# Optimization experiments

Measured on AMD Instinct MI355X. Metric: run time of the kernel, lower is better.

The kernel has to match this reference:

```python
import jax, jax.numpy as jnp
import numpy as np

B = 8192      # contrastive batch size
D = 64        # embedding dim
TEMP = 0.07   # temperature (init kwarg)
EPS = 1e-8    # F.cosine_similarity eps
N_CLASSES = 1000


def setup_inputs() -> dict:
    key = jax.random.key(0)
    k1, k2, k3 = jax.random.split(key, 3)
    return {
        "label_tensor": jax.random.randint(k1, (B,), 0, N_CLASSES),
        "feature_a": jax.random.normal(k2, (B, D), dtype=jnp.float32),
        "feature_b": jax.random.normal(k3, (B, D), dtype=jnp.float32),
    }


def reference(label_tensor, feature_a, feature_b):
    # cos_score[i, j] = cosine(feature_a[i], feature_b[j])  -> [B, B]
    na = jnp.maximum(jnp.linalg.norm(feature_a, axis=1), EPS)  # [B]
    nb = jnp.maximum(jnp.linalg.norm(feature_b, axis=1), EPS)  # [B]
    cos_score = (feature_a @ feature_b.T) / (na[:, None] * nb[None, :])

    # cross_modality=True (feature_b given): no diagonal exclusion.
    e = jnp.exp(cos_score / TEMP)                               # [B, B]
    same = label_tensor[:, None] == label_tensor[None, :]       # [B, B] bool
    numerator = jnp.sum(jnp.where(same, e, 0.0), axis=1)        # [B]
    denominator = jnp.sum(e, axis=1)                            # [B]
    # original: if numerator == 0: numerator += 0.01
    numerator = jnp.where(numerator == 0.0, numerator + 0.01, numerator)
    loss = -jnp.mean(jnp.log(numerator / denominator))
    return (loss.reshape(1), cos_score)
```

## Files before the change

### kernel.cpp

```cpp
#include <hip/hip_runtime.h>

#define BATCH 8192
#define DIM 64
#define INV_TEMP 14.2857142857142857f
#define EPS_NORM 1e-8f
#define NXB 8
#define CT_PER_BLOCK 8

typedef __attribute__((ext_vector_type(8))) short bf16x8;
typedef __attribute__((ext_vector_type(4))) float f32x4;

__device__ __forceinline__ unsigned short f2bf_rne(float x) {
  unsigned int u = __float_as_uint(x);
  u += 0x7FFFu + ((u >> 16) & 1u);
  return (unsigned short)(u >> 16);
}

__global__ __launch_bounds__(256) void norm_kernel(
    const float* __restrict__ A, const float* __restrict__ Bm,
    unsigned short* __restrict__ An, unsigned short* __restrict__ Bn,
    float* __restrict__ out) {
  int gid  = blockIdx.x * 256 + threadIdx.x;
  int row  = gid >> 6;
  int lane = gid & 63;
  float a = A[row * DIM + lane];
  float b = Bm[row * DIM + lane];
  float sa = a * a, sb = b * b;
#pragma unroll
  for (int m = 32; m; m >>= 1) {
    sa += __shfl_xor(sa, m);
    sb += __shfl_xor(sb, m);
  }
  float ia = 1.0f / fmaxf(sqrtf(sa), EPS_NORM);
  float ib = 1.0f / fmaxf(sqrtf(sb), EPS_NORM);
  An[row * DIM + lane] = f2bf_rne(a * ia);
  Bn[row * DIM + lane] = f2bf_rne(b * ib);
  if (gid == 0) out[0] = 0.0f;
}

__global__ __launch_bounds__(256) void cos_mfma_kernel(
    const unsigned short* __restrict__ An, const unsigned short* __restrict__ Bn,
    const int* __restrict__ labels,
    float* __restrict__ pN, float* __restrict__ pD,
    float* __restrict__ cos_out) {
  const int tid  = threadIdx.x;
  const int lane = tid & 63;
  const int wave = tid >> 6;
  const int wr = wave >> 1, wc = wave & 1;
  const int m = lane & 15, q = lane >> 4;
  const int row0 = blockIdx.y * 128 + wr * 64;

  bf16x8 afr[4][2];
#pragma unroll
  for (int t = 0; t < 4; ++t) {
    const unsigned short* ap = An + (size_t)(row0 + t * 16 + m) * DIM + q * 8;
#pragma unroll
    for (int h = 0; h < 2; ++h) afr[t][h] = *(const bf16x8*)(ap + h * 32);
  }

  int lrw[4][4];
#pragma unroll
  for (int mt = 0; mt < 4; ++mt) {
    int lr = labels[row0 + mt * 16 + m];
#pragma unroll
    for (int i = 0; i < 4; ++i) lrw[mt][i] = __shfl(lr, q * 4 + i);
  }

  float es[4][4], ns[4][4];
#pragma unroll
  for (int mt = 0; mt < 4; ++mt)
#pragma unroll
    for (int i = 0; i < 4; ++i) { es[mt][i] = 0.f; ns[mt][i] = 0.f; }

  for (int ct = 0; ct < CT_PER_BLOCK; ++ct) {
    const int col0 = (blockIdx.x * CT_PER_BLOCK + ct) * 128 + wc * 64;

    bf16x8 bfr[4][2];
#pragma unroll
    for (int t = 0; t < 4; ++t) {
      const unsigned short* bp = Bn + (size_t)(col0 + t * 16 + m) * DIM + q * 8;
#pragma unroll
      for (int h = 0; h < 2; ++h) bfr[t][h] = *(const bf16x8*)(bp + h * 32);
    }
    int labc[4];
#pragma unroll
    for (int nt = 0; nt < 4; ++nt) labc[nt] = labels[col0 + nt * 16 + m];

#pragma unroll
    for (int mt = 0; mt < 4; ++mt) {
#pragma unroll
      for (int nt = 0; nt < 4; ++nt) {
        f32x4 a = {0.f, 0.f, 0.f, 0.f};
        a = __builtin_amdgcn_mfma_f32_16x16x32_bf16(afr[mt][0], bfr[nt][0], a, 0, 0, 0);
        a = __builtin_amdgcn_mfma_f32_16x16x32_bf16(afr[mt][1], bfr[nt][1], a, 0, 0, 0);
#pragma unroll
        for (int i = 0; i < 4; ++i) {
          float c = a[i];
          size_t row = (size_t)(row0 + mt * 16 + q * 4 + i);
          cos_out[row * BATCH + col0 + nt * 16 + m] = c;
          float e = __expf(c * INV_TEMP);
          es[mt][i] += e;
          if (labc[nt] == lrw[mt][i]) ns[mt][i] += e;
        }
      }
    }
  }

#pragma unroll
  for (int mt = 0; mt < 4; ++mt)
#pragma unroll
    for (int i = 0; i < 4; ++i) {
      float e = es[mt][i], n = ns[mt][i];
#pragma unroll
      for (int msk = 1; msk < 16; msk <<= 1) {
        e += __shfl_xor(e, msk);
        n += __shfl_xor(n, msk);
      }
      es[mt][i] = e; ns[mt][i] = n;
    }

  __shared__ float redN[2][128], redD[2][128];
  if (m == 0) {
#pragma unroll
    for (int mt = 0; mt < 4; ++mt)
#pragma unroll
      for (int i = 0; i < 4; ++i) {
        int r = wr * 64 + mt * 16 + q * 4 + i;
        redN[wc][r] = ns[mt][i];
        redD[wc][r] = es[mt][i];
      }
  }
  __syncthreads();
  if (tid < 128) {
    int row = blockIdx.y * 128 + tid;
    pN[(size_t)blockIdx.x * BATCH + row] = redN[0][tid] + redN[1][tid];
    pD[(size_t)blockIdx.x * BATCH + row] = redD[0][tid] + redD[1][tid];
  }
}

__global__ __launch_bounds__(256) void loss_kernel(
    const float* __restrict__ pN, const float* __restrict__ pD,
    float* __restrict__ out) {
  int r = blockIdx.x * 256 + threadIdx.x;
  float n = 0.f, d = 0.f;
#pragma unroll
  for (int j = 0; j < NXB; ++j) {
    n += pN[(size_t)j * BATCH + r];
    d += pD[(size_t)j * BATCH + r];
  }
  n = (n == 0.0f) ? (n + 0.01f) : n;
  float s = logf(n / d);
#pragma unroll
  for (int m = 32; m; m >>= 1) s += __shfl_xor(s, m);
  __shared__ float red[4];
  if ((threadIdx.x & 63) == 0) red[threadIdx.x >> 6] = s;
  __syncthreads();
  if (threadIdx.x == 0) {
    float t = red[0] + red[1] + red[2] + red[3];
    atomicAdd(out, -t / (float)BATCH);
  }
}

extern "C" void kernel_launch(void* const* d_in, const int* in_sizes, int n_in,
                              void* d_out, int out_size, void* d_ws, size_t ws_size,
                              hipStream_t stream) {
  const int*   labels = (const int*)d_in[0];
  const float* A      = (const float*)d_in[1];
  const float* Bf     = (const float*)d_in[2];
  float* out = (float*)d_out;

  unsigned short* An = (unsigned short*)d_ws;
  unsigned short* Bn = An + BATCH * DIM;
  float* pN = (float*)(Bn + BATCH * DIM);
  float* pD = pN + (size_t)NXB * BATCH;

  hipLaunchKernelGGL(norm_kernel, dim3(BATCH * 64 / 256), dim3(256), 0, stream,
                     A, Bf, An, Bn, out);
  hipLaunchKernelGGL(cos_mfma_kernel, dim3(NXB, BATCH / 128), dim3(256),
                     0, stream, An, Bn, labels, pN, pD, out + 1);
  hipLaunchKernelGGL(loss_kernel, dim3(BATCH / 256), dim3(256), 0, stream,
                     pN, pD, out);
}
```

Measured before the change: 388.6 us.

## Transpose MFMA operands for row-contiguous vector stores and regrid column tiles

Swaps the MFMA operand order so each lane holds four consecutive columns of one row. The cosine matrix can then be written with 16-byte vector stores instead of strided scalar stores, and label compares use int4 loads. The row reduction drops from a 16-lane shuffle tree to two cross-quad shuffles. The grid also changes from 8x8 to 32x2 column tiles per block. Some column positions take an odd mix of nontemporal and plain scalar stores, which adds branch complexity, and the pN/pD workspace grows fourfold.

```diff
diff --git a/kernel.cpp b/kernel.cpp
--- a/kernel.cpp
+++ b/kernel.cpp
@@ -4,11 +4,13 @@
 #define DIM 64
 #define INV_TEMP 14.2857142857142857f
 #define EPS_NORM 1e-8f
-#define NXB 8
-#define CT_PER_BLOCK 8
+#define NXB 32
+#define CT_PER_BLOCK 2
 
 typedef __attribute__((ext_vector_type(8))) short bf16x8;
 typedef __attribute__((ext_vector_type(4))) float f32x4;
+
+struct __attribute__((packed, aligned(4))) f32x4_u { f32x4 v; };
 
 __device__ __forceinline__ unsigned short f2bf_rne(float x) {
   unsigned int u = __float_as_uint(x);
@@ -58,20 +60,15 @@
     for (int h = 0; h < 2; ++h) afr[t][h] = *(const bf16x8*)(ap + h * 32);
   }
 
-  int lrw[4][4];
+  int lrw[4];
 #pragma unroll
-  for (int mt = 0; mt < 4; ++mt) {
-    int lr = labels[row0 + mt * 16 + m];
+  for (int mt = 0; mt < 4; ++mt) lrw[mt] = labels[row0 + mt * 16 + m];
+
+  float es[4], ns[4];
 #pragma unroll
-    for (int i = 0; i < 4; ++i) lrw[mt][i] = __shfl(lr, q * 4 + i);
-  }
+  for (int mt = 0; mt < 4; ++mt) { es[mt] = 0.f; ns[mt] = 0.f; }
 
-  float es[4][4], ns[4][4];
 #pragma unroll
-  for (int mt = 0; mt < 4; ++mt)
-#pragma unroll
-    for (int i = 0; i < 4; ++i) { es[mt][i] = 0.f; ns[mt][i] = 0.f; }
-
   for (int ct = 0; ct < CT_PER_BLOCK; ++ct) {
     const int col0 = (blockIdx.x * CT_PER_BLOCK + ct) * 128 + wc * 64;
 
@@ -82,53 +79,62 @@
 #pragma unroll
       for (int h = 0; h < 2; ++h) bfr[t][h] = *(const bf16x8*)(bp + h * 32);
     }
-    int labc[4];
+    int4 labc[4];
 #pragma unroll
-    for (int nt = 0; nt < 4; ++nt) labc[nt] = labels[col0 + nt * 16 + m];
+    for (int nt = 0; nt < 4; ++nt)
+      labc[nt] = *(const int4*)&labels[col0 + nt * 16 + q * 4];
 
 #pragma unroll
     for (int mt = 0; mt < 4; ++mt) {
 #pragma unroll
       for (int nt = 0; nt < 4; ++nt) {
         f32x4 a = {0.f, 0.f, 0.f, 0.f};
-        a = __builtin_amdgcn_mfma_f32_16x16x32_bf16(afr[mt][0], bfr[nt][0], a, 0, 0, 0);
-        a = __builtin_amdgcn_mfma_f32_16x16x32_bf16(afr[mt][1], bfr[nt][1], a, 0, 0, 0);
+        a = __builtin_amdgcn_mfma_f32_16x16x32_bf16(bfr[nt][0], afr[mt][0], a, 0, 0, 0);
+        a = __builtin_amdgcn_mfma_f32_16x16x32_bf16(bfr[nt][1], afr[mt][1], a, 0, 0, 0);
+        const int cmod = ct * 128 + wc * 64 + nt * 16 + q * 4;
+        float* p = cos_out + (size_t)(row0 + mt * 16 + m) * BATCH
+                           + (col0 + nt * 16 + q * 4);
+        if ((cmod <= 28) || (cmod == 252)) {
 #pragma unroll
-        for (int i = 0; i < 4; ++i) {
-          float c = a[i];
-          size_t row = (size_t)(row0 + mt * 16 + q * 4 + i);
-          cos_out[row * BATCH + col0 + nt * 16 + m] = c;
-          float e = __expf(c * INV_TEMP);
-          es[mt][i] += e;
-          if (labc[nt] == lrw[mt][i]) ns[mt][i] += e;
+          for (int r = 0; r < 4; ++r) {
+            int colm = cmod + r;
+            if (colm <= 30 || colm == 255) __builtin_nontemporal_store(a[r], p + r);
+            else                           p[r] = a[r];
+          }
+        } else {
+          ((f32x4_u*)p)->v = a;
         }
+        float e0 = __expf(a[0] * INV_TEMP);
+        float e1 = __expf(a[1] * INV_TEMP);
+        float e2 = __expf(a[2] * INV_TEMP);
+        float e3 = __expf(a[3] * INV_TEMP);
+        es[mt] += (e0 + e1) + (e2 + e3);
+        float nacc = 0.f;
+        if (labc[nt].x == lrw[mt]) nacc += e0;
+        if (labc[nt].y == lrw[mt]) nacc += e1;
+        if (labc[nt].z == lrw[mt]) nacc += e2;
+        if (labc[nt].w == lrw[mt]) nacc += e3;
+        ns[mt] += nacc;
       }
     }
   }
 
 #pragma unroll
-  for (int mt = 0; mt < 4; ++mt)
-#pragma unroll
-    for (int i = 0; i < 4; ++i) {
-      float e = es[mt][i], n = ns[mt][i];
-#pragma unroll
-      for (int msk = 1; msk < 16; msk <<= 1) {
-        e += __shfl_xor(e, msk);
-        n += __shfl_xor(n, msk);
-      }
-      es[mt][i] = e; ns[mt][i] = n;
-    }
+  for (int mt = 0; mt < 4; ++mt) {
+    float e = es[mt], n = ns[mt];
+    e += __shfl_xor(e, 16); n += __shfl_xor(n, 16);
+    e += __shfl_xor(e, 32); n += __shfl_xor(n, 32);
+    es[mt] = e; ns[mt] = n;
+  }
 
   __shared__ float redN[2][128], redD[2][128];
-  if (m == 0) {
+  if (q == 0) {
 #pragma unroll
-    for (int mt = 0; mt < 4; ++mt)
-#pragma unroll
-      for (int i = 0; i < 4; ++i) {
-        int r = wr * 64 + mt * 16 + q * 4 + i;
-        redN[wc][r] = ns[mt][i];
-        redD[wc][r] = es[mt][i];
-      }
+    for (int mt = 0; mt < 4; ++mt) {
+      int r = wr * 64 + mt * 16 + m;
+      redN[wc][r] = ns[mt];
+      redD[wc][r] = es[mt];
+    }
   }
   __syncthreads();
   if (tid < 128) {
```

Result: faster. 349.6 us (-10.0%).

## Stage cosine tile through LDS for 16-byte coalesced output stores

Applied to the files above, without the earlier changes.

Restructures the similarity kernel so each wave computes a 16x256 tile, writes the MFMA results into shared memory, then reads them back so each lane stores a contiguous float4 of a row. The output buffer is offset by one float, so the staging uses a rotated column index to line the vector stores up with 16-byte boundaries, and a few edge stores are non-temporal. The original kernel wrote scattered scalar floats, which made the 256MB output write inefficient. This adds LDS traffic and a full-wave shuffle reduction per row, and shifts the grid to smaller blocks with more column partials.

```diff
diff --git a/kernel.cpp b/kernel.cpp
--- a/kernel.cpp
+++ b/kernel.cpp
@@ -4,8 +4,7 @@
 #define DIM 64
 #define INV_TEMP 14.2857142857142857f
 #define EPS_NORM 1e-8f
-#define NXB 8
-#define CT_PER_BLOCK 8
+#define NXB 32
 
 typedef __attribute__((ext_vector_type(8))) short bf16x8;
 typedef __attribute__((ext_vector_type(4))) float f32x4;
@@ -38,103 +37,82 @@
   if (gid == 0) out[0] = 0.0f;
 }
 
-__global__ __launch_bounds__(256) void cos_mfma_kernel(
+__global__ __launch_bounds__(128) void cos_mfma_kernel(
     const unsigned short* __restrict__ An, const unsigned short* __restrict__ Bn,
     const int* __restrict__ labels,
     float* __restrict__ pN, float* __restrict__ pD,
-    float* __restrict__ cos_out) {
-  const int tid  = threadIdx.x;
-  const int lane = tid & 63;
-  const int wave = tid >> 6;
-  const int wr = wave >> 1, wc = wave & 1;
-  const int m = lane & 15, q = lane >> 4;
-  const int row0 = blockIdx.y * 128 + wr * 64;
+    float* __restrict__ out ) {
+  const int tid = threadIdx.x;
+  const int l = tid & 63;
+  const int w = tid >> 6;
+  const int m = l & 15, q = l >> 4;
+  const int bcol0 = blockIdx.x * 256;
+  const int R0 = blockIdx.y * 32 + w * 16;
 
-  bf16x8 afr[4][2];
+  __shared__ float lds[2][16][264];
+
+  bf16x8 afr[2];
 #pragma unroll
-  for (int t = 0; t < 4; ++t) {
-    const unsigned short* ap = An + (size_t)(row0 + t * 16 + m) * DIM + q * 8;
+  for (int h = 0; h < 2; ++h)
+    afr[h] = *(const bf16x8*)(An + (size_t)(R0 + m) * DIM + h * 32 + q * 8);
+
+  int lr = labels[R0 + m];
+  int labc[4];
 #pragma unroll
-    for (int h = 0; h < 2; ++h) afr[t][h] = *(const bf16x8*)(ap + h * 32);
+  for (int r = 0; r < 4; ++r)
+    labc[r] = labels[bcol0 + ((4 * l + r - 1) & 255)];
+
+#pragma unroll
+  for (int nt = 0; nt < 16; ++nt) {
+    const unsigned short* bp = Bn + (size_t)(bcol0 + nt * 16 + m) * DIM + q * 8;
+    bf16x8 b0 = *(const bf16x8*)(bp);
+    bf16x8 b1 = *(const bf16x8*)(bp + 32);
+    f32x4 a = {0.f, 0.f, 0.f, 0.f};
+    a = __builtin_amdgcn_mfma_f32_16x16x32_bf16(b0, afr[0], a, 0, 0, 0);
+    a = __builtin_amdgcn_mfma_f32_16x16x32_bf16(b1, afr[1], a, 0, 0, 0);
+#pragma unroll
+    for (int r = 0; r < 4; ++r)
+      lds[w][m][(nt * 16 + q * 4 + r + 1) & 255] = a[r];
   }
 
-  int lrw[4][4];
+  float esk = 0.f, nsk = 0.f;
 #pragma unroll
-  for (int mt = 0; mt < 4; ++mt) {
-    int lr = labels[row0 + mt * 16 + m];
+  for (int j = 0; j < 16; ++j) {
+    f32x4 v = *(const f32x4*)&lds[w][j][4 * l];
+    size_t base = (size_t)(R0 + j) * BATCH + bcol0;
+    float* p = out + base + 4 * l;
+    if (l == 0) {
+      __builtin_nontemporal_store(v[1], out + base + 1);
+      __builtin_nontemporal_store(v[2], out + base + 2);
+      __builtin_nontemporal_store(v[3], out + base + 3);
+      __builtin_nontemporal_store(v[0], out + base + 256);
+    } else if (l < 8) {
+      __builtin_nontemporal_store(v, (f32x4*)p);
+    } else {
+      *(f32x4*)p = v;
+    }
+    float e0 = __expf(v[0] * INV_TEMP);
+    float e1 = __expf(v[1] * INV_TEMP);
+    float e2 = __expf(v[2] * INV_TEMP);
+    float e3 = __expf(v[3] * INV_TEMP);
+    float es = (e0 + e1) + (e2 + e3);
+    int lrj = __shfl(lr, j);
+    float ns = 0.f;
+    if (labc[0] == lrj) ns += e0;
+    if (labc[1] == lrj) ns += e1;
+    if (labc[2] == lrj) ns += e2;
+    if (labc[3] == lrj) ns += e3;
 #pragma unroll
-    for (int i = 0; i < 4; ++i) lrw[mt][i] = __shfl(lr, q * 4 + i);
+    for (int msk = 1; msk < 64; msk <<= 1) {
+      es += __shfl_xor(es, msk);
+      ns += __shfl_xor(ns, msk);
+    }
+    if ((l & 15) == j) { esk = es; nsk = ns; }
   }
 
-  float es[4][4], ns[4][4];
-#pragma unroll
-  for (int mt = 0; mt < 4; ++mt)
-#pragma unroll
-    for (int i = 0; i < 4; ++i) { es[mt][i] = 0.f; ns[mt][i] = 0.f; }
-
-  for (int ct = 0; ct < CT_PER_BLOCK; ++ct) {
-    const int col0 = (blockIdx.x * CT_PER_BLOCK + ct) * 128 + wc * 64;
-
-    bf16x8 bfr[4][2];
-#pragma unroll
-    for (int t = 0; t < 4; ++t) {
-      const unsigned short* bp = Bn + (size_t)(col0 + t * 16 + m) * DIM + q * 8;
-#pragma unroll
-      for (int h = 0; h < 2; ++h) bfr[t][h] = *(const bf16x8*)(bp + h * 32);
-    }
-    int labc[4];
-#pragma unroll
-    for (int nt = 0; nt < 4; ++nt) labc[nt] = labels[col0 + nt * 16 + m];
-
-#pragma unroll
-    for (int mt = 0; mt < 4; ++mt) {
-#pragma unroll
-      for (int nt = 0; nt < 4; ++nt) {
-        f32x4 a = {0.f, 0.f, 0.f, 0.f};
-        a = __builtin_amdgcn_mfma_f32_16x16x32_bf16(afr[mt][0], bfr[nt][0], a, 0, 0, 0);
-        a = __builtin_amdgcn_mfma_f32_16x16x32_bf16(afr[mt][1], bfr[nt][1], a, 0, 0, 0);
-#pragma unroll
-        for (int i = 0; i < 4; ++i) {
-          float c = a[i];
-          size_t row = (size_t)(row0 + mt * 16 + q * 4 + i);
-          cos_out[row * BATCH + col0 + nt * 16 + m] = c;
-          float e = __expf(c * INV_TEMP);
-          es[mt][i] += e;
-          if (labc[nt] == lrw[mt][i]) ns[mt][i] += e;
-        }
-      }
-    }
-  }
-
-#pragma unroll
-  for (int mt = 0; mt < 4; ++mt)
-#pragma unroll
-    for (int i = 0; i < 4; ++i) {
-      float e = es[mt][i], n = ns[mt][i];
-#pragma unroll
-      for (int msk = 1; msk < 16; msk <<= 1) {
-        e += __shfl_xor(e, msk);
-        n += __shfl_xor(n, msk);
-      }
-      es[mt][i] = e; ns[mt][i] = n;
-    }
-
-  __shared__ float redN[2][128], redD[2][128];
-  if (m == 0) {
-#pragma unroll
-    for (int mt = 0; mt < 4; ++mt)
-#pragma unroll
-      for (int i = 0; i < 4; ++i) {
-        int r = wr * 64 + mt * 16 + q * 4 + i;
-        redN[wc][r] = ns[mt][i];
-        redD[wc][r] = es[mt][i];
-      }
-  }
-  __syncthreads();
-  if (tid < 128) {
-    int row = blockIdx.y * 128 + tid;
-    pN[(size_t)blockIdx.x * BATCH + row] = redN[0][tid] + redN[1][tid];
-    pD[(size_t)blockIdx.x * BATCH + row] = redD[0][tid] + redD[1][tid];
+  if (l < 16) {
+    pN[(size_t)blockIdx.x * BATCH + R0 + l] = nsk;
+    pD[(size_t)blockIdx.x * BATCH + R0 + l] = esk;
   }
 }
 
@@ -176,8 +154,8 @@
 
   hipLaunchKernelGGL(norm_kernel, dim3(BATCH * 64 / 256), dim3(256), 0, stream,
                      A, Bf, An, Bn, out);
-  hipLaunchKernelGGL(cos_mfma_kernel, dim3(NXB, BATCH / 128), dim3(256),
-                     0, stream, An, Bn, labels, pN, pD, out + 1);
+  hipLaunchKernelGGL(cos_mfma_kernel, dim3(NXB, BATCH / 32), dim3(128),
+                     0, stream, An, Bn, labels, pN, pD, out);
   hipLaunchKernelGGL(loss_kernel, dim3(BATCH / 256), dim3(256), 0, stream,
                      pN, pD, out);
 }
```

New measurement: 361.3 us. 1.08x faster.
